# Performance work log

Hardware: AMD Instinct MI355X
Metric: run time of the kernel (lower is better)

## Reference

```python
import jax, jax.numpy as jnp
import numpy as np

B, S, D = 2, 2048, 4096
NH, NKV = 32, 8
HD = D // NH          # 128
NREP = NH // NKV      # 4 (GQA groups)


def _rope(t, cos, sin):
    # t: [b, s, h, d]; cos/sin: [s, d//2]; interleaved (real, imag) pairs on last dim
    tr = t.reshape(*t.shape[:-1], -1, 2)
    a, b = tr[..., 0], tr[..., 1]
    c = cos[None, :, None, :]
    s = sin[None, :, None, :]
    out = jnp.stack([a * c - b * s, a * s + b * c], axis=-1)
    return out.reshape(t.shape)


def _repeat_kv(t, n_rep):
    # [b, s, n_kv, d] -> [b, s, n_kv*n_rep, d]
    b, s, nkv, d = t.shape
    return jnp.broadcast_to(t[:, :, :, None, :], (b, s, nkv, n_rep, d)).reshape(b, s, nkv * n_rep, d)


def setup_inputs() -> dict:
    key = jax.random.key(0)
    ks = jax.random.split(key, 5)
    x = jax.random.normal(ks[0], (B, S, D), jnp.float32)
    wq = jax.random.normal(ks[1], (D, NH * HD), jnp.float32) * 0.02
    wk = jax.random.normal(ks[2], (D, NKV * HD), jnp.float32) * 0.02
    wv = jax.random.normal(ks[3], (D, NKV * HD), jnp.float32) * 0.02
    wo = jax.random.normal(ks[4], (NH * HD, D), jnp.float32) * 0.02
    inv_freq = 1.0 / (10000.0 ** (jnp.arange(0, HD, 2, dtype=jnp.float32) / HD))
    angles = jnp.arange(S, dtype=jnp.float32)[:, None] * inv_freq[None, :]  # [S, HD//2]
    return {
        "x": x, "wq": wq, "wk": wk, "wv": wv, "wo": wo,
        "freqs_cos": jnp.cos(angles), "freqs_sin": jnp.sin(angles),
        "start_pos": 0,
    }


def reference(x, wq, wk, wv, wo, freqs_cos, freqs_sin, start_pos):
    b, s, _ = x.shape
    xq = (x @ wq).reshape(b, s, NH, HD)
    xk = (x @ wk).reshape(b, s, NKV, HD)
    xv = (x @ wv).reshape(b, s, NKV, HD)
    xq = _rope(xq, freqs_cos, freqs_sin)
    xk = _rope(xk, freqs_cos, freqs_sin)
    # prefill (start_pos=0): cache[:b, :s] = xk/xv, then keys/values read back equal xk/xv
    keys = _repeat_kv(xk, NREP)    # [b, s, NH, HD]
    values = _repeat_kv(xv, NREP)  # [b, s, NH, HD]
    scores = jnp.einsum("bqhd,bkhd->bhqk", xq, keys) / jnp.sqrt(jnp.float32(HD))
    probs = jax.nn.softmax(scores, axis=-1)
    out = jnp.einsum("bhqk,bkhd->bqhd", probs, values).reshape(b, s, NH * HD)
    return out @ wo
```

## Files before the change

kernel.cpp:

```cpp
#include <hip/hip_runtime.h>
#include <hip/hip_bf16.h>
#include <cstdint>

#define B_   2
#define S_   2048
#define D_   4096
#define NH_  32
#define NKV_ 8
#define HD_  128
#define BS_  (B_*S_)
#define NQK_ 6144

typedef __bf16 bf16_t;
typedef __bf16 bf16x8 __attribute__((ext_vector_type(8)));
typedef __bf16 bf16x4 __attribute__((ext_vector_type(4)));
typedef __bf16 bf16x2 __attribute__((ext_vector_type(2)));
typedef float  f32x4  __attribute__((ext_vector_type(4)));
typedef float  f32x16 __attribute__((ext_vector_type(16)));
typedef unsigned uint32x4 __attribute__((ext_vector_type(4)));

typedef const __attribute__((address_space(1))) void* gas_ptr;
typedef __attribute__((address_space(3))) void* las_ptr;

__device__ __forceinline__ void gload_lds16(const void* g, void* l) {
  __builtin_amdgcn_global_load_lds((gas_ptr)g, (las_ptr)l, 16, 0, 0);
}

__device__ __forceinline__ float exp2_fast(float x) {
  float r;
  asm("v_exp_f32 %0, %1" : "=v"(r) : "v"(x));
  return r;
}

__device__ __forceinline__ unsigned cvt_pk_bf16(float a, float b) {
  unsigned r;
  asm("v_cvt_pk_bf16_f32 %0, %1, %2" : "=v"(r) : "v"(a), "v"(b));
  return r;
}

#define LD8(p) (*(const bf16x8*)(p))
#define MFMA(a, b, c) __builtin_amdgcn_mfma_f32_16x16x32_bf16(a, b, c, 0, 0, 0)
#define MFMA32(a, b, c) __builtin_amdgcn_mfma_f32_32x32x16_bf16(a, b, c, 0, 0, 0)

__global__ __launch_bounds__(256) void k_cvt(const float4* __restrict__ in,
                                             bf16x4* __restrict__ out, int n4) {
  int i = blockIdx.x * 256 + threadIdx.x;
  if (i >= n4) return;
  float4 v = in[i];
  bf16x4 o = { (bf16_t)v.x, (bf16_t)v.y, (bf16_t)v.z, (bf16_t)v.w };
  out[i] = o;
}

__global__ __launch_bounds__(256) void k_transpose_cvt(const float* __restrict__ w,
                                                       bf16_t* __restrict__ wt,
                                                       int K, int N) {
  __shared__ float tile[32][33];
  int n0 = blockIdx.x * 32, k0 = blockIdx.y * 32;
  int tx = threadIdx.x, ty = threadIdx.y;
#pragma unroll
  for (int i = 0; i < 4; i++)
    tile[ty + 8*i][tx] = w[(size_t)(k0 + ty + 8*i) * N + n0 + tx];
  __syncthreads();
#pragma unroll
  for (int i = 0; i < 4; i++)
    wt[(size_t)(n0 + ty + 8*i) * K + k0 + tx] = (bf16_t)tile[tx][ty + 8*i];
}

template <typename CT>
__global__ __launch_bounds__(512, 2) void k_gemm8p(const bf16_t* __restrict__ A,
                                                   const bf16_t* __restrict__ Bt,
                                                   CT* __restrict__ C,
                                                   int M, int N, int K, int KL,
                                                   long long zsC) {
  constexpr int NF = 4;
  __shared__ __align__(16) bf16_t As[2][256 * 64];
  __shared__ __align__(16) bf16_t Bs[2][NF * 64 * 64];
  const int tid = threadIdx.x;
  const int l = tid & 63, w = tid >> 6;
  const int lr = l & 15, lg = l >> 4;
  const int wm = w >> 2, wn = w & 3;

  const int bm = blockIdx.x, bn = blockIdx.y;
  const int kOff = blockIdx.z * KL;

  const bf16_t* Ab = A  + (size_t)bm * 256 * K + kOff;
  const bf16_t* Bb = Bt + (size_t)bn * 256 * K + kOff;
  C += (long long)blockIdx.z * zsC;

  int st_row[4], st_col[4], st_dst[4];
#pragma unroll
  for (int j = 0; j < 4; j++) {
    int o = (j * 512 + tid) * 16;
    int row = o >> 7, cb = o & 127;
    st_row[j] = row;
    st_col[j] = (cb ^ ((row & 7) << 4)) >> 1;
    st_dst[j] = o >> 1;
  }

  int aoff[8], boff[NF];
#pragma unroll
  for (int m = 0; m < 8; m++) {
    int r = wm * 128 + m * 16 + lr;
    aoff[m] = r * 64 + (((lg * 16) ^ ((r & 7) << 4)) >> 1);
  }
#pragma unroll
  for (int n = 0; n < NF; n++) {
    int r = wn * 64 + n * 16 + lr;
    boff[n] = r * 64 + (((lg * 16) ^ ((r & 7) << 4)) >> 1);
  }

  f32x4 acc[8][NF];
#pragma unroll
  for (int m = 0; m < 8; m++)
#pragma unroll
    for (int n = 0; n < NF; n++) acc[m][n] = f32x4{0.f, 0.f, 0.f, 0.f};

  auto stageA = [&](int k, int h) {
    const int kt = k << 6;
    const int rof = h << 7;
#pragma unroll
    for (int j = 0; j < 2; j++)
      gload_lds16(Ab + (size_t)(st_row[j] + rof) * K + kt + st_col[j],
                  &As[k & 1][0] + (rof << 6) + st_dst[j]);
  };
  auto stageB = [&](int k) {
    const int kt = k << 6;
#pragma unroll
    for (int j = 0; j < NF; j++)
      gload_lds16(Bb + (size_t)st_row[j] * K + kt + st_col[j],
                  &Bs[k & 1][0] + st_dst[j]);
  };

  const int NT = KL >> 6;
  stageA(0, 0); stageA(0, 1); stageB(0); stageB(1);
  asm volatile("s_waitcnt vmcnt(4)" ::: "memory");
  __builtin_amdgcn_s_barrier();

  for (int k = 0; k < NT; ++k) {
    const bf16_t* Ap = &As[k & 1][0];
    const bf16_t* Bp = &Bs[k & 1][0];
    const bool s1 = (k + 1 < NT), s2 = (k + 2 < NT);
    bf16x8 bfr[NF], a[4];

#pragma unroll
    for (int n = 0; n < NF; n++) bfr[n] = LD8(Bp + boff[n]);
#pragma unroll
    for (int m = 0; m < 4; m++) a[m] = LD8(Ap + aoff[m]);
    if (s1) stageA(k + 1, 0);
    __builtin_amdgcn_s_barrier();
    asm volatile("s_waitcnt lgkmcnt(0)" ::: "memory");
    __builtin_amdgcn_s_setprio(1);
#pragma unroll
    for (int m = 0; m < 4; m++)
#pragma unroll
      for (int n = 0; n < NF; n++)
        acc[m][n] = MFMA(a[m], bfr[n], acc[m][n]);
    __builtin_amdgcn_s_setprio(0);
    __builtin_amdgcn_s_barrier();

#pragma unroll
    for (int m = 0; m < 4; m++) a[m] = LD8(Ap + aoff[m + 4]);
    if (s1) stageA(k + 1, 1);
    __builtin_amdgcn_s_barrier();
    asm volatile("s_waitcnt lgkmcnt(0)" ::: "memory");
    __builtin_amdgcn_s_setprio(1);
#pragma unroll
    for (int m = 0; m < 4; m++)
#pragma unroll
      for (int n = 0; n < NF; n++)
        acc[m + 4][n] = MFMA(a[m], bfr[n], acc[m + 4][n]);
    __builtin_amdgcn_s_setprio(0);
    __builtin_amdgcn_s_barrier();

#pragma unroll
    for (int n = 0; n < NF; n++) bfr[n] = LD8(Bp + (boff[n] ^ 32));
#pragma unroll
    for (int m = 0; m < 4; m++) a[m] = LD8(Ap + (aoff[m] ^ 32));
    __builtin_amdgcn_s_barrier();
    asm volatile("s_waitcnt lgkmcnt(0)" ::: "memory");
    __builtin_amdgcn_s_setprio(1);
#pragma unroll
    for (int m = 0; m < 4; m++)
#pragma unroll
      for (int n = 0; n < NF; n++)
        acc[m][n] = MFMA(a[m], bfr[n], acc[m][n]);
    __builtin_amdgcn_s_setprio(0);
    __builtin_amdgcn_s_barrier();

#pragma unroll
    for (int m = 0; m < 4; m++) a[m] = LD8(Ap + (aoff[m + 4] ^ 32));
    if (s2) {
      stageB(k + 2);
      asm volatile("s_waitcnt vmcnt(4)" ::: "memory");
    } else if (s1) {
      asm volatile("s_waitcnt vmcnt(0)" ::: "memory");
    }
    __builtin_amdgcn_s_barrier();
    asm volatile("s_waitcnt lgkmcnt(0)" ::: "memory");
    __builtin_amdgcn_s_setprio(1);
#pragma unroll
    for (int m = 0; m < 4; m++)
#pragma unroll
      for (int n = 0; n < NF; n++)
        acc[m + 4][n] = MFMA(a[m], bfr[n], acc[m + 4][n]);
    __builtin_amdgcn_s_setprio(0);
    __builtin_amdgcn_s_barrier();
  }

#pragma unroll
  for (int m = 0; m < 8; m++) {
    int row0 = bm * 256 + wm * 128 + m * 16 + lg * 4;
#pragma unroll
    for (int n = 0; n < NF; n++) {
      int col = bn * 256 + wn * 64 + n * 16 + lr;
#pragma unroll
      for (int i = 0; i < 4; i++)
        C[(size_t)(row0 + i) * N + col] = (CT)acc[m][n][i];
    }
  }
}

__global__ __launch_bounds__(256) void k_rope(const bf16_t* __restrict__ s1,
                                              const bf16_t* __restrict__ s2,
                                              const float* __restrict__ fcos,
                                              const float* __restrict__ fsin,
                                              bf16_t* __restrict__ dst,
                                              int nheads, int stride, float mul) {
  int idx = blockIdx.x * 256 + threadIdx.x;
  int p = idx & 63;
  int h = (idx >> 6) % nheads;
  int bs = idx / (64 * nheads);
  int s = bs & (S_ - 1);
  int b = bs >> 11;
  size_t off = (size_t)bs * stride + h * HD_ + 2 * p;
  bf16x2 ab = *(const bf16x2*)(s1 + off);
  float a = (float)ab[0], bb = (float)ab[1];
  if (s2) {
    bf16x2 ab2 = *(const bf16x2*)(s2 + off);
    a += (float)ab2[0]; bb += (float)ab2[1];
  }
  float c = fcos[s * 64 + p], sn = fsin[s * 64 + p];
  bf16x2 o = { (bf16_t)((a * c - bb * sn) * mul), (bf16_t)((a * sn + bb * c) * mul) };
  *(bf16x2*)(dst + ((((size_t)b * nheads + h) * S_ + s) * HD_) + 2 * p) = o;
}

__global__ __launch_bounds__(256) void k_vtrans(const bf16_t* __restrict__ pA,
                                                const bf16_t* __restrict__ pB,
                                                bf16_t* __restrict__ vtr) {
  __shared__ bf16_t tile[32][33];
  int s0 = blockIdx.x * 32, d0 = blockIdx.y * 32, z = blockIdx.z;
  int b = z >> 3, kvh = z & 7;
  int tx = threadIdx.x, ty = threadIdx.y;
#pragma unroll
  for (int i = 0; i < 4; i++) {
    size_t off = (size_t)(b * S_ + s0 + ty + 8*i) * 2048 + 1024 + kvh * HD_ + d0 + tx;
    tile[ty + 8*i][tx] = (bf16_t)((float)pA[off] + (float)pB[off]);
  }
  __syncthreads();
#pragma unroll
  for (int i = 0; i < 4; i++)
    vtr[((size_t)z * HD_ + d0 + ty + 8*i) * S_ + s0 + tx] = tile[tx][ty + 8*i];
}

#define KVBLK 64
#define SM_THR 12.0f
__global__ __launch_bounds__(256, 2) void k_flash(const bf16_t* __restrict__ qr,
                                                  const bf16_t* __restrict__ kr,
                                                  const bf16_t* __restrict__ vt,
                                                  bf16_t* __restrict__ ctx) {
  __shared__ __align__(16) bf16_t Ks[2][KVBLK * HD_];
  __shared__ __align__(16) bf16_t Vs[2][64 * 128];
  const int tid = threadIdx.x;
  const int l = tid & 63, w = tid >> 6;
  const int q5 = l & 31, h = l >> 5;
  const int qb = blockIdx.x, hh = blockIdx.y, b = blockIdx.z;
  const int kvh = hh >> 2;

  const bf16_t* qbase = qr + (((size_t)b * NH_ + hh) * S_ + qb * 128 + w * 32) * HD_;
  const bf16_t* kbase = kr + (((size_t)b * NKV_ + kvh) * S_) * HD_;
  const bf16_t* vbase = vt + (((size_t)b * NKV_ + kvh) * HD_) * S_;

  bf16x8 qf[8];
#pragma unroll
  for (int s = 0; s < 8; s++)
    qf[s] = LD8(qbase + q5 * HD_ + s * 16 + h * 8);

  f32x16 acco[4];
#pragma unroll
  for (int db = 0; db < 4; db++)
#pragma unroll
    for (int r = 0; r < 16; r++) acco[db][r] = 0.f;
  float mR = -1e30f, lR = 0.f;

  auto stage = [&](int bu, int t) {
    const int kb = t * KVBLK;
#pragma unroll
    for (int j = 0; j < 4; j++) {
      int o_ = (tid + 256 * j) * 16;
      int row = o_ >> 8, cb = o_ & 255;
      int scb = cb ^ ((row & 15) << 4);
      gload_lds16(kbase + (size_t)(kb + row) * HD_ + (scb >> 1),
                  &Ks[bu][0] + (o_ >> 1));
    }
#pragma unroll
    for (int j = 0; j < 4; j++) {
      int o_ = (tid + 256 * j) * 16;
      int row = o_ >> 8, cb = o_ & 255;
      int sin_ = cb ^ ((row & 15) << 4);
      int d = 2 * row + (sin_ >> 7);
      int s0 = (sin_ & 127) >> 1;
      gload_lds16(vbase + (size_t)d * S_ + kb + s0,
                  &Vs[bu][0] + (o_ >> 1));
    }
  };

  const int nt = S_ / KVBLK;
  stage(0, 0);
  __syncthreads();
  int buf = 0;

  for (int t = 0; t < nt; t++) {
    if (t + 1 < nt) stage(buf ^ 1, t + 1);
    const bf16_t* Kb = &Ks[buf][0];
    const bf16_t* Vb = &Vs[buf][0];

    f32x16 accs[2];
#pragma unroll
    for (int kb = 0; kb < 2; kb++)
#pragma unroll
      for (int r = 0; r < 16; r++) accs[kb][r] = 0.f;
    __builtin_amdgcn_s_setprio(1);
#pragma unroll
    for (int s = 0; s < 8; s++) {
#pragma unroll
      for (int kb = 0; kb < 2; kb++) {
        int r = kb * 32 + q5;
        int cb = (32 * s + 16 * h) ^ ((r & 15) << 4);
        bf16x8 kf = LD8(Kb + (r << 7) + (cb >> 1));
        accs[kb] = MFMA32(kf, qf[s], accs[kb]);
      }
    }
    __builtin_amdgcn_s_setprio(0);

    float lm = accs[0][0];
#pragma unroll
    for (int kb = 0; kb < 2; kb++)
#pragma unroll
      for (int r = 0; r < 16; r++)
        if (kb | r) lm = fmaxf(lm, accs[kb][r]);
    if (!__all(lm - mR <= SM_THR)) {
      float fm = fmaxf(lm, __shfl_xor(lm, 32));
      float mnew = fmaxf(mR, fm);
      float alpha = exp2_fast(mR - mnew);
      mR = mnew;
      lR *= alpha;
#pragma unroll
      for (int db = 0; db < 4; db++)
#pragma unroll
        for (int r = 0; r < 16; r++) acco[db][r] *= alpha;
    }
    float psum = 0.f;
    bf16x8 pb[4];
#pragma unroll
    for (int s2 = 0; s2 < 4; s2++) {
      const int kb = s2 >> 1, rb = (s2 & 1) * 8;
      float pv[8];
#pragma unroll
      for (int j = 0; j < 8; j++) {
        pv[j] = exp2_fast(accs[kb][rb + j] - mR);
        psum += pv[j];
      }
      unsigned wlo0 = cvt_pk_bf16(pv[0], pv[1]);
      unsigned wlo1 = cvt_pk_bf16(pv[2], pv[3]);
      unsigned whi0 = cvt_pk_bf16(pv[4], pv[5]);
      unsigned whi1 = cvt_pk_bf16(pv[6], pv[7]);
      asm volatile("v_permlane32_swap_b32 %0, %1" : "+v"(wlo0), "+v"(whi0));
      asm volatile("v_permlane32_swap_b32 %0, %1" : "+v"(wlo1), "+v"(whi1));
      uint32x4 wv = { wlo0, wlo1, whi0, whi1 };
      pb[s2] = __builtin_bit_cast(bf16x8, wv);
    }
    psum += __shfl_xor(psum, 32);
    lR += psum;

    __builtin_amdgcn_s_setprio(1);
#pragma unroll
    for (int s2 = 0; s2 < 4; s2++) {
#pragma unroll
      for (int db = 0; db < 4; db++) {
        int rv = db * 32 + q5;
        int row = rv >> 1;
        int cb = (((rv & 1) << 7) | (32 * s2 + 16 * h)) ^ ((row & 15) << 4);
        bf16x8 vf = LD8(Vb + (row << 7) + (cb >> 1));
        acco[db] = MFMA32(vf, pb[s2], acco[db]);
      }
    }
    __builtin_amdgcn_s_setprio(0);
    __syncthreads();
    buf ^= 1;
  }

  float inv = 1.0f / lR;
  bf16_t* tb = &Ks[0][0] + w * (32 * 128);
#pragma unroll
  for (int db = 0; db < 4; db++)
#pragma unroll
    for (int rp = 0; rp < 8; rp++) {
      int r = 2 * rp;
      int d0 = (r & 3) + 8 * (r >> 2) + 4 * h + 32 * db;
      unsigned word = cvt_pk_bf16(acco[db][r] * inv, acco[db][r + 1] * inv);
      int cbyte = (d0 * 2) ^ ((q5 & 15) << 4);
      *(unsigned*)((char*)tb + q5 * 256 + cbyte) = word;
    }
  __syncthreads();
#pragma unroll
  for (int it = 0; it < 8; it++) {
    int gid = it * 256 + tid;
    int wv = gid >> 9, rem = gid & 511;
    int qq = rem >> 4, g = rem & 15;
    int cbyte = (g * 16) ^ ((qq & 15) << 4);
    bf16x8 v = LD8((const bf16_t*)((const char*)(&Ks[0][0] + wv * (32 * 128)) + qq * 256 + cbyte));
    int srow = qb * 128 + wv * 32 + qq;
    *(bf16x8*)(ctx + ((size_t)(b * S_ + srow)) * D_ + hh * HD_ + g * 8) = v;
  }
}

extern "C" void kernel_launch(void* const* d_in, const int* in_sizes, int n_in,
                              void* d_out, int out_size, void* d_ws, size_t ws_size,
                              hipStream_t stream) {
  const float* x    = (const float*)d_in[0];
  const float* wq   = (const float*)d_in[1];
  const float* wk   = (const float*)d_in[2];
  const float* wv   = (const float*)d_in[3];
  const float* wo   = (const float*)d_in[4];
  const float* fcos = (const float*)d_in[5];
  const float* fsin = (const float*)d_in[6];
  float* out = (float*)d_out;

  const size_t MB = 1u << 20;
  char* p = (char*)d_ws;
  bf16_t* xb    = (bf16_t*)p;
  bf16_t* wqkvt = (bf16_t*)(p + 32 * MB);
  bf16_t* wot   = (bf16_t*)(p + 80 * MB);
  bf16_t* qc    = (bf16_t*)(p + 112 * MB);
  bf16_t* partA = (bf16_t*)(p + 144 * MB);
  bf16_t* partB = wot;
  bf16_t* qrope = xb;
  bf16_t* krope = wqkvt;
  bf16_t* vtr   = wqkvt + (size_t)BS_ * NKV_ * HD_;
  bf16_t* ctx   = qc;

  const float QSCALE = (float)(0.08838834764831845 * 1.4426950408889634);

  dim3 tb(32, 8);
  k_cvt<<<BS_ * D_ / 1024, 256, 0, stream>>>((const float4*)x, (bf16x4*)xb, BS_ * D_ / 4);
  k_transpose_cvt<<<dim3(D_ / 32, D_ / 32), tb, 0, stream>>>(wq, wqkvt, D_, D_);
  k_transpose_cvt<<<dim3(32, D_ / 32), tb, 0, stream>>>(wk, wqkvt + (size_t)D_ * D_, D_, NKV_ * HD_);
  k_transpose_cvt<<<dim3(32, D_ / 32), tb, 0, stream>>>(wv, wqkvt + (size_t)(D_ + NKV_ * HD_) * D_, D_, NKV_ * HD_);
  k_gemm8p<bf16_t><<<dim3(BS_ / 256, D_ / 256, 1), 512, 0, stream>>>(
      xb, wqkvt, qc, BS_, D_, D_, D_, 0);
  k_gemm8p<bf16_t><<<dim3(BS_ / 256, 2048 / 256, 2), 512, 0, stream>>>(
      xb, wqkvt + (size_t)D_ * D_, partA, BS_, 2048, D_, 2048,
      (long long)(partB - partA));
  k_rope<<<BS_ * NH_ * 64 / 256, 256, 0, stream>>>(qc, (const bf16_t*)nullptr,
      fcos, fsin, qrope, NH_, D_, QSCALE);
  k_rope<<<BS_ * NKV_ * 64 / 256, 256, 0, stream>>>(partA, partB,
      fcos, fsin, krope, NKV_, 2048, 1.0f);
  k_vtrans<<<dim3(S_ / 32, HD_ / 32, B_ * NKV_), tb, 0, stream>>>(partA, partB, vtr);
  k_transpose_cvt<<<dim3(D_ / 32, D_ / 32), tb, 0, stream>>>(wo, wot, D_, D_);
  k_flash<<<dim3(S_ / 128, NH_, B_), 256, 0, stream>>>(qrope, krope, vtr, ctx);
  k_gemm8p<float><<<dim3(BS_ / 256, D_ / 256, 1), 512, 0, stream>>>(
      ctx, wot, out, BS_, D_, D_, D_, 0);
}
```

Measured before the change: 568.1 us.

## Double query rows per wave in flash attention to reuse K/V fragments

Each wave now processes two 32-row query tiles (64 rows), so every K and V fragment loaded from LDS feeds two MFMAs, and each block covers 256 queries. This halves LDS reads per unit of attention work and halves the number of K/V tile loads from global memory. In exchange, register use roughly doubles for accumulators and Q fragments, launch bounds drop to one block per CU, and the grid halves, reducing occupancy and latency hiding.

Result: slower. 588.9 us (+3.7%).

```diff
diff --git a/kernel.cpp b/kernel.cpp
--- a/kernel.cpp
+++ b/kernel.cpp
@@ -264,33 +264,36 @@
 
 #define KVBLK 64
 #define SM_THR 12.0f
-__global__ __launch_bounds__(256, 2) void k_flash(const bf16_t* __restrict__ qr,
+__global__ __launch_bounds__(256, 1) void k_flash(const bf16_t* __restrict__ qr,
                                                   const bf16_t* __restrict__ kr,
                                                   const bf16_t* __restrict__ vt,
                                                   bf16_t* __restrict__ ctx) {
-  __shared__ __align__(16) bf16_t Ks[2][KVBLK * HD_];
-  __shared__ __align__(16) bf16_t Vs[2][64 * 128];
+  __shared__ __align__(16) bf16_t smem[32768];
   const int tid = threadIdx.x;
   const int l = tid & 63, w = tid >> 6;
   const int q5 = l & 31, h = l >> 5;
   const int qb = blockIdx.x, hh = blockIdx.y, b = blockIdx.z;
   const int kvh = hh >> 2;
 
-  const bf16_t* qbase = qr + (((size_t)b * NH_ + hh) * S_ + qb * 128 + w * 32) * HD_;
+  const bf16_t* qbase = qr + (((size_t)b * NH_ + hh) * S_ + qb * 256 + w * 64) * HD_;
   const bf16_t* kbase = kr + (((size_t)b * NKV_ + kvh) * S_) * HD_;
   const bf16_t* vbase = vt + (((size_t)b * NKV_ + kvh) * HD_) * S_;
 
-  bf16x8 qf[8];
-#pragma unroll
-  for (int s = 0; s < 8; s++)
-    qf[s] = LD8(qbase + q5 * HD_ + s * 16 + h * 8);
-
-  f32x16 acco[4];
-#pragma unroll
-  for (int db = 0; db < 4; db++)
-#pragma unroll
-    for (int r = 0; r < 16; r++) acco[db][r] = 0.f;
-  float mR = -1e30f, lR = 0.f;
+  bf16x8 qf[2][8];
+#pragma unroll
+  for (int m = 0; m < 2; m++)
+#pragma unroll
+    for (int s = 0; s < 8; s++)
+      qf[m][s] = LD8(qbase + (m * 32 + q5) * HD_ + s * 16 + h * 8);
+
+  f32x16 acco[2][4];
+#pragma unroll
+  for (int m = 0; m < 2; m++)
+#pragma unroll
+    for (int db = 0; db < 4; db++)
+#pragma unroll
+      for (int r = 0; r < 16; r++) acco[m][db][r] = 0.f;
+  float mR[2] = {-1e30f, -1e30f}, lR[2] = {0.f, 0.f};
 
   auto stage = [&](int bu, int t) {
     const int kb = t * KVBLK;
@@ -300,7 +303,7 @@
       int row = o_ >> 8, cb = o_ & 255;
       int scb = cb ^ ((row & 15) << 4);
       gload_lds16(kbase + (size_t)(kb + row) * HD_ + (scb >> 1),
-                  &Ks[bu][0] + (o_ >> 1));
+                  smem + bu * 8192 + (o_ >> 1));
     }
 #pragma unroll
     for (int j = 0; j < 4; j++) {
@@ -310,7 +313,7 @@
       int d = 2 * row + (sin_ >> 7);
       int s0 = (sin_ & 127) >> 1;
       gload_lds16(vbase + (size_t)d * S_ + kb + s0,
-                  &Vs[bu][0] + (o_ >> 1));
+                  smem + 16384 + bu * 8192 + (o_ >> 1));
     }
   };
 
@@ -321,14 +324,16 @@
 
   for (int t = 0; t < nt; t++) {
     if (t + 1 < nt) stage(buf ^ 1, t + 1);
-    const bf16_t* Kb = &Ks[buf][0];
-    const bf16_t* Vb = &Vs[buf][0];
-
-    f32x16 accs[2];
-#pragma unroll
-    for (int kb = 0; kb < 2; kb++)
-#pragma unroll
-      for (int r = 0; r < 16; r++) accs[kb][r] = 0.f;
+    const bf16_t* Kb = smem + buf * 8192;
+    const bf16_t* Vb = smem + 16384 + buf * 8192;
+
+    f32x16 accs[2][2];
+#pragma unroll
+    for (int m = 0; m < 2; m++)
+#pragma unroll
+      for (int kb = 0; kb < 2; kb++)
+#pragma unroll
+        for (int r = 0; r < 16; r++) accs[m][kb][r] = 0.f;
     __builtin_amdgcn_s_setprio(1);
 #pragma unroll
     for (int s = 0; s < 8; s++) {
@@ -337,50 +342,54 @@
         int r = kb * 32 + q5;
         int cb = (32 * s + 16 * h) ^ ((r & 15) << 4);
         bf16x8 kf = LD8(Kb + (r << 7) + (cb >> 1));
-        accs[kb] = MFMA32(kf, qf[s], accs[kb]);
+        accs[0][kb] = MFMA32(kf, qf[0][s], accs[0][kb]);
+        accs[1][kb] = MFMA32(kf, qf[1][s], accs[1][kb]);
       }
     }
     __builtin_amdgcn_s_setprio(0);
 
-    float lm = accs[0][0];
-#pragma unroll
-    for (int kb = 0; kb < 2; kb++)
-#pragma unroll
-      for (int r = 0; r < 16; r++)
-        if (kb | r) lm = fmaxf(lm, accs[kb][r]);
-    if (!__all(lm - mR <= SM_THR)) {
-      float fm = fmaxf(lm, __shfl_xor(lm, 32));
-      float mnew = fmaxf(mR, fm);
-      float alpha = exp2_fast(mR - mnew);
-      mR = mnew;
-      lR *= alpha;
-#pragma unroll
-      for (int db = 0; db < 4; db++)
-#pragma unroll
-        for (int r = 0; r < 16; r++) acco[db][r] *= alpha;
-    }
-    float psum = 0.f;
-    bf16x8 pb[4];
-#pragma unroll
-    for (int s2 = 0; s2 < 4; s2++) {
-      const int kb = s2 >> 1, rb = (s2 & 1) * 8;
-      float pv[8];
-#pragma unroll
-      for (int j = 0; j < 8; j++) {
-        pv[j] = exp2_fast(accs[kb][rb + j] - mR);
-        psum += pv[j];
+    bf16x8 pb[2][4];
+#pragma unroll
+    for (int m = 0; m < 2; m++) {
+      float lm = accs[m][0][0];
+#pragma unroll
+      for (int kb = 0; kb < 2; kb++)
+#pragma unroll
+        for (int r = 0; r < 16; r++)
+          if (kb | r) lm = fmaxf(lm, accs[m][kb][r]);
+      if (!__all(lm - mR[m] <= SM_THR)) {
+        float fm = fmaxf(lm, __shfl_xor(lm, 32));
+        float mnew = fmaxf(mR[m], fm);
+        float alpha = exp2_fast(mR[m] - mnew);
+        mR[m] = mnew;
+        lR[m] *= alpha;
+#pragma unroll
+        for (int db = 0; db < 4; db++)
+#pragma unroll
+          for (int r = 0; r < 16; r++) acco[m][db][r] *= alpha;
       }
-      unsigned wlo0 = cvt_pk_bf16(pv[0], pv[1]);
-      unsigned wlo1 = cvt_pk_bf16(pv[2], pv[3]);
-      unsigned whi0 = cvt_pk_bf16(pv[4], pv[5]);
-      unsigned whi1 = cvt_pk_bf16(pv[6], pv[7]);
-      asm volatile("v_permlane32_swap_b32 %0, %1" : "+v"(wlo0), "+v"(whi0));
-      asm volatile("v_permlane32_swap_b32 %0, %1" : "+v"(wlo1), "+v"(whi1));
-      uint32x4 wv = { wlo0, wlo1, whi0, whi1 };
-      pb[s2] = __builtin_bit_cast(bf16x8, wv);
-    }
-    psum += __shfl_xor(psum, 32);
-    lR += psum;
+      float psum = 0.f;
+#pragma unroll
+      for (int s2 = 0; s2 < 4; s2++) {
+        const int kb = s2 >> 1, rb = (s2 & 1) * 8;
+        float pv[8];
+#pragma unroll
+        for (int j = 0; j < 8; j++) {
+          pv[j] = exp2_fast(accs[m][kb][rb + j] - mR[m]);
+          psum += pv[j];
+        }
+        unsigned wlo0 = cvt_pk_bf16(pv[0], pv[1]);
+        unsigned wlo1 = cvt_pk_bf16(pv[2], pv[3]);
+        unsigned whi0 = cvt_pk_bf16(pv[4], pv[5]);
+        unsigned whi1 = cvt_pk_bf16(pv[6], pv[7]);
+        asm volatile("v_permlane32_swap_b32 %0, %1" : "+v"(wlo0), "+v"(whi0));
+        asm volatile("v_permlane32_swap_b32 %0, %1" : "+v"(wlo1), "+v"(whi1));
+        uint32x4 wv = { wlo0, wlo1, whi0, whi1 };
+        pb[m][s2] = __builtin_bit_cast(bf16x8, wv);
+      }
+      psum += __shfl_xor(psum, 32);
+      lR[m] += psum;
+    }
 
     __builtin_amdgcn_s_setprio(1);
 #pragma unroll
@@ -391,7 +400,8 @@
         int row = rv >> 1;
         int cb = (((rv & 1) << 7) | (32 * s2 + 16 * h)) ^ ((row & 15) << 4);
         bf16x8 vf = LD8(Vb + (row << 7) + (cb >> 1));
-        acco[db] = MFMA32(vf, pb[s2], acco[db]);
+        acco[0][db] = MFMA32(vf, pb[0][s2], acco[0][db]);
+        acco[1][db] = MFMA32(vf, pb[1][s2], acco[1][db]);
       }
     }
     __builtin_amdgcn_s_setprio(0);
@@ -399,27 +409,29 @@
     buf ^= 1;
   }
 
-  float inv = 1.0f / lR;
-  bf16_t* tb = &Ks[0][0] + w * (32 * 128);
-#pragma unroll
-  for (int db = 0; db < 4; db++)
-#pragma unroll
-    for (int rp = 0; rp < 8; rp++) {
-      int r = 2 * rp;
-      int d0 = (r & 3) + 8 * (r >> 2) + 4 * h + 32 * db;
-      unsigned word = cvt_pk_bf16(acco[db][r] * inv, acco[db][r + 1] * inv);
-      int cbyte = (d0 * 2) ^ ((q5 & 15) << 4);
-      *(unsigned*)((char*)tb + q5 * 256 + cbyte) = word;
-    }
+#pragma unroll
+  for (int m = 0; m < 2; m++) {
+    float inv = 1.0f / lR[m];
+    char* tb = (char*)smem + (w * 64 + m * 32) * 256;
+#pragma unroll
+    for (int db = 0; db < 4; db++)
+#pragma unroll
+      for (int rp = 0; rp < 8; rp++) {
+        int r = 2 * rp;
+        int d0 = (r & 3) + 8 * (r >> 2) + 4 * h + 32 * db;
+        unsigned word = cvt_pk_bf16(acco[m][db][r] * inv, acco[m][db][r + 1] * inv);
+        int cbyte = (d0 * 2) ^ ((q5 & 15) << 4);
+        *(unsigned*)(tb + q5 * 256 + cbyte) = word;
+      }
+  }
   __syncthreads();
 #pragma unroll
-  for (int it = 0; it < 8; it++) {
+  for (int it = 0; it < 16; it++) {
     int gid = it * 256 + tid;
-    int wv = gid >> 9, rem = gid & 511;
-    int qq = rem >> 4, g = rem & 15;
+    int qq = gid >> 4, g = gid & 15;
     int cbyte = (g * 16) ^ ((qq & 15) << 4);
-    bf16x8 v = LD8((const bf16_t*)((const char*)(&Ks[0][0] + wv * (32 * 128)) + qq * 256 + cbyte));
-    int srow = qb * 128 + wv * 32 + qq;
+    bf16x8 v = LD8((const bf16_t*)((const char*)smem + qq * 256 + cbyte));
+    int srow = qb * 256 + qq;
     *(bf16x8*)(ctx + ((size_t)(b * S_ + srow)) * D_ + hh * HD_ + g * 8) = v;
   }
 }
@@ -467,7 +479,7 @@
       fcos, fsin, krope, NKV_, 2048, 1.0f);
   k_vtrans<<<dim3(S_ / 32, HD_ / 32, B_ * NKV_), tb, 0, stream>>>(partA, partB, vtr);
   k_transpose_cvt<<<dim3(D_ / 32, D_ / 32), tb, 0, stream>>>(wo, wot, D_, D_);
-  k_flash<<<dim3(S_ / 128, NH_, B_), 256, 0, stream>>>(qrope, krope, vtr, ctx);
+  k_flash<<<dim3(S_ / 256, NH_, B_), 256, 0, stream>>>(qrope, krope, vtr, ctx);
   k_gemm8p<float><<<dim3(BS_ / 256, D_ / 256, 1), 512, 0, stream>>>(
       ctx, wot, out, BS_, D_, D_, D_, 0);
 }
```
